# Kernel tuning notes

Measured on AMD Instinct MI355X. Metric: run time of the kernel, lower is better.

Reference implementation:

```python
import jax, jax.numpy as jnp
import numpy as np

B, M, N = 256, 256, 256

def setup_inputs() -> dict:
    key = jax.random.key(0)
    k1, k2 = jax.random.split(key)
    x_real = jax.random.normal(k1, (B, M, N), dtype=jnp.float32)
    x_imag = jax.random.normal(k2, (B, M, N), dtype=jnp.float32)
    return {"x_real": x_real, "x_imag": x_imag}

def reference(x_real, x_imag):
    # complex k-space input; original used complex128 via numpy on host,
    # we use complex64 (the natural accelerator precision), same math.
    x = jax.lax.complex(x_real, x_imag)  # [B, M, N]
    axes = (-2, -1)
    # centered 2D IFFT per sample (ifft_along_dim): fftshift(ifft2(ifftshift(x)))
    y = jnp.fft.fftshift(jnp.fft.ifft2(jnp.fft.ifftshift(x, axes=axes), axes=axes), axes=axes)
    y = y.reshape(-1, 1, M, N)  # (-1, 1, M, N) as in call()
    return (jnp.real(y), jnp.imag(y))
```

## Files before the change

kernel.cpp:

```cpp
#include <hip/hip_runtime.h>

namespace {

constexpr int NN  = 256;
constexpr int BMN = 256 * 256 * 256;

struct cpx { float re, im; };

__device__ __forceinline__ cpx cadd(cpx a, cpx b){ return cpx{a.re + b.re, a.im + b.im}; }
__device__ __forceinline__ cpx csub(cpx a, cpx b){ return cpx{a.re - b.re, a.im - b.im}; }
__device__ __forceinline__ cpx cmul(cpx a, cpx b){ return cpx{a.re*b.re - a.im*b.im, a.re*b.im + a.im*b.re}; }
__device__ __forceinline__ cpx cmuli(cpx a){ return cpx{-a.im, a.re}; }

__device__ __forceinline__ void r4(cpx a, cpx b, cpx c, cpx d,
                                   cpx& y0, cpx& y1, cpx& y2, cpx& y3) {
  cpx apc = cadd(a, c), amc = csub(a, c);
  cpx bpd = cadd(b, d), bmd = csub(b, d);
  cpx ib  = cmuli(bmd);
  y0 = cadd(apc, bpd);
  y1 = cadd(amc, ib);
  y2 = csub(apc, bpd);
  y3 = csub(amc, ib);
}

__device__ __forceinline__ void ifft16(cpx x[16]) {
  constexpr float WC[10] = { 1.f,  0.9238795325112867f,  0.7071067811865476f,  0.3826834323650898f, 0.f,
                            -0.3826834323650898f, -0.7071067811865476f, -0.9238795325112867f, -1.f,
                            -0.9238795325112867f };
  constexpr float WS[10] = { 0.f,  0.3826834323650898f,  0.7071067811865476f,  0.9238795325112867f, 1.f,
                             0.9238795325112867f,  0.7071067811865476f,  0.3826834323650898f,  0.f,
                            -0.3826834323650898f };
  cpx B[4][4];
#pragma unroll
  for (int n1 = 0; n1 < 4; ++n1)
    r4(x[n1], x[n1 + 4], x[n1 + 8], x[n1 + 12],
       B[n1][0], B[n1][1], B[n1][2], B[n1][3]);
#pragma unroll
  for (int n1 = 1; n1 < 4; ++n1)
#pragma unroll
    for (int k2 = 1; k2 < 4; ++k2)
      B[n1][k2] = cmul(B[n1][k2], cpx{WC[n1 * k2], WS[n1 * k2]});
#pragma unroll
  for (int k2 = 0; k2 < 4; ++k2)
    r4(B[0][k2], B[1][k2], B[2][k2], B[3][k2],
       x[k2], x[k2 + 4], x[k2 + 8], x[k2 + 12]);
}

__device__ __forceinline__ void twiddle256(cpx a[16], int t) {
  const float base = 0.024543692606170259f * (float)t;
#pragma unroll
  for (int k1 = 1; k1 < 16; ++k1) {
    float s, c;
    __sincosf(base * (float)k1, &s, &c);
    a[k1] = cmul(a[k1], cpx{c, s});
  }
}

__device__ __forceinline__ void transpose16(cpx a[16], float* L, int t) {
#pragma unroll
  for (int k1 = 0; k1 < 16; ++k1) L[k1 * 17 + t] = a[k1].re;
  __syncthreads();
  float br[16];
#pragma unroll
  for (int n2 = 0; n2 < 16; ++n2) br[n2] = L[t * 17 + n2];
  __syncthreads();
#pragma unroll
  for (int k1 = 0; k1 < 16; ++k1) L[k1 * 17 + t] = a[k1].im;
  __syncthreads();
#pragma unroll
  for (int n2 = 0; n2 < 16; ++n2) { a[n2].im = L[t * 17 + n2]; a[n2].re = br[n2]; }
}

__global__ __launch_bounds__(256)
void k_ifft_rows(const float* __restrict__ xr, const float* __restrict__ xi,
                 float* __restrict__ yr, float* __restrict__ yi) {
  __shared__ float lbuf[16 * 273];
  const int tid  = threadIdx.x;
  const int t    = tid & 15;
  const int ll   = tid >> 4;
  const int line = blockIdx.x * 16 + ll;
  const float* pr = xr + line * NN;
  const float* pi = xi + line * NN;

  cpx a[16];
#pragma unroll
  for (int j = 0; j < 16; ++j) {
    const int idx = (((j << 4) | t) ^ 128);
    a[j] = cpx{ pr[idx], pi[idx] };
  }
  ifft16(a);
  twiddle256(a, t);

  transpose16(a, lbuf + ll * 273, t);

  ifft16(a);
  float* qr = yr + line * NN;
  float* qi = yi + line * NN;
#pragma unroll
  for (int k = 0; k < 16; ++k) {
    const int idx = (((k << 4) | t) ^ 128);
    qr[idx] = a[k].re;
    qi[idx] = a[k].im;
  }
}

__global__ __launch_bounds__(512)
void k_ifft_cols(float* __restrict__ yr, float* __restrict__ yi) {
  __shared__ float lbuf[32 * 273];
  const int tid = threadIdx.x;
  const int c   = tid & 31;
  const int t   = tid >> 5;
  const int b   = blockIdx.x >> 3;
  const int c0  = (blockIdx.x & 7) << 5;
  const int base = b * 65536 + c0 + c;

  cpx a[16];
#pragma unroll
  for (int j = 0; j < 16; ++j) {
    const int m = (((j << 4) | t) ^ 128);
    a[j] = cpx{ yr[base + m * NN], yi[base + m * NN] };
  }
  ifft16(a);
  twiddle256(a, t);

  transpose16(a, lbuf + c * 273, t);

  ifft16(a);
  constexpr float sc = 1.0f / 65536.0f;
#pragma unroll
  for (int k = 0; k < 16; ++k) {
    const int m = (((k << 4) | t) ^ 128);
    yr[base + m * NN] = a[k].re * sc;
    yi[base + m * NN] = a[k].im * sc;
  }
}

}

extern "C" void kernel_launch(void* const* d_in, const int* in_sizes, int n_in,
                              void* d_out, int out_size, void* d_ws, size_t ws_size,
                              hipStream_t stream) {
  const float* xr = (const float*)d_in[0];
  const float* xi = (const float*)d_in[1];
  float* yr = (float*)d_out;
  float* yi = yr + BMN;

  k_ifft_rows<<<4096, 256, 0, stream>>>(xr, xi, yr, yi);
  k_ifft_cols<<<2048, 512, 0, stream>>>(yr, yi);
}
```

Baseline: 86.95 us.

## Stage row-FFT loads and stores through LDS with float4 coalesced access

The row kernel now loads its 16 lines with coalesced float4 global reads into padded shared buffers for real and imaginary parts, then gathers the shifted strided elements from LDS. Output goes back through LDS and is written with float4 stores. The internal transpose uses separate real/imag buffers, cutting one barrier round-trip. The aim is to replace strided 4-byte global accesses with wide coalesced ones, at the cost of more LDS traffic and extra barriers. The column kernel only has its transpose helper inlined.

```diff
diff --git a/kernel.cpp b/kernel.cpp
--- a/kernel.cpp
+++ b/kernel.cpp
@@ -2,8 +2,9 @@
 
 namespace {
 
-constexpr int NN  = 256;
-constexpr int BMN = 256 * 256 * 256;
+constexpr int NN   = 256;
+constexpr int BMN  = 256 * 256 * 256;
+constexpr int LPAD = 272;
 
 struct cpx { float re, im; };
 
@@ -56,51 +57,76 @@
   }
 }
 
-__device__ __forceinline__ void transpose16(cpx a[16], float* L, int t) {
-#pragma unroll
-  for (int k1 = 0; k1 < 16; ++k1) L[k1 * 17 + t] = a[k1].re;
-  __syncthreads();
-  float br[16];
-#pragma unroll
-  for (int n2 = 0; n2 < 16; ++n2) br[n2] = L[t * 17 + n2];
-  __syncthreads();
-#pragma unroll
-  for (int k1 = 0; k1 < 16; ++k1) L[k1 * 17 + t] = a[k1].im;
-  __syncthreads();
-#pragma unroll
-  for (int n2 = 0; n2 < 16; ++n2) { a[n2].im = L[t * 17 + n2]; a[n2].re = br[n2]; }
-}
-
 __global__ __launch_bounds__(256)
 void k_ifft_rows(const float* __restrict__ xr, const float* __restrict__ xi,
                  float* __restrict__ yr, float* __restrict__ yi) {
-  __shared__ float lbuf[16 * 273];
-  const int tid  = threadIdx.x;
-  const int t    = tid & 15;
-  const int ll   = tid >> 4;
-  const int line = blockIdx.x * 16 + ll;
-  const float* pr = xr + line * NN;
-  const float* pi = xi + line * NN;
+  __shared__ float Lr[16 * LPAD];
+  __shared__ float Li[16 * LPAD];
+  const int tid = threadIdx.x;
+  const int t   = tid & 15;
+  const int ll  = tid >> 4;
+
+  const size_t blk = (size_t)blockIdx.x * (16 * NN);
+  const float4* sr4 = reinterpret_cast<const float4*>(xr + blk);
+  const float4* si4 = reinterpret_cast<const float4*>(xi + blk);
+
+#pragma unroll
+  for (int q = 0; q < 4; ++q) {
+    const int fi   = (q << 8) + tid;
+    const int line = fi >> 6;
+    const int slot = fi & 63;
+    *reinterpret_cast<float4*>(&Lr[line * LPAD + slot * 4]) = sr4[fi];
+    *reinterpret_cast<float4*>(&Li[line * LPAD + slot * 4]) = si4[fi];
+  }
+  __syncthreads();
 
   cpx a[16];
+  {
+    const float* lr = Lr + ll * LPAD;
+    const float* li = Li + ll * LPAD;
 #pragma unroll
-  for (int j = 0; j < 16; ++j) {
-    const int idx = (((j << 4) | t) ^ 128);
-    a[j] = cpx{ pr[idx], pi[idx] };
+    for (int j = 0; j < 16; ++j) {
+      const int idx = (((j << 4) | t) ^ 128);
+      a[j] = cpx{ lr[idx], li[idx] };
+    }
   }
   ifft16(a);
   twiddle256(a, t);
+  __syncthreads();
 
-  transpose16(a, lbuf + ll * 273, t);
+  {
+    float* lr = Lr + ll * LPAD;
+    float* li = Li + ll * LPAD;
+#pragma unroll
+    for (int k1 = 0; k1 < 16; ++k1) { lr[k1 * 17 + t] = a[k1].re; li[k1 * 17 + t] = a[k1].im; }
+    __syncthreads();
+#pragma unroll
+    for (int n2 = 0; n2 < 16; ++n2) { a[n2].re = lr[t * 17 + n2]; a[n2].im = li[t * 17 + n2]; }
+  }
+  ifft16(a);
+  __syncthreads();
 
-  ifft16(a);
-  float* qr = yr + line * NN;
-  float* qi = yi + line * NN;
+  {
+    float* lr = Lr + ll * LPAD;
+    float* li = Li + ll * LPAD;
 #pragma unroll
-  for (int k = 0; k < 16; ++k) {
-    const int idx = (((k << 4) | t) ^ 128);
-    qr[idx] = a[k].re;
-    qi[idx] = a[k].im;
+    for (int k = 0; k < 16; ++k) {
+      const int idx = (((k << 4) | t) ^ 128);
+      lr[idx] = a[k].re;
+      li[idx] = a[k].im;
+    }
+  }
+  __syncthreads();
+
+  float4* dr4 = reinterpret_cast<float4*>(yr + blk);
+  float4* di4 = reinterpret_cast<float4*>(yi + blk);
+#pragma unroll
+  for (int q = 0; q < 4; ++q) {
+    const int fi   = (q << 8) + tid;
+    const int line = fi >> 6;
+    const int slot = fi & 63;
+    dr4[fi] = *reinterpret_cast<const float4*>(&Lr[line * LPAD + slot * 4]);
+    di4[fi] = *reinterpret_cast<const float4*>(&Li[line * LPAD + slot * 4]);
   }
 }
 
@@ -123,7 +149,21 @@
   ifft16(a);
   twiddle256(a, t);
 
-  transpose16(a, lbuf + c * 273, t);
+  {
+    float* L = lbuf + c * 273;
+#pragma unroll
+    for (int k1 = 0; k1 < 16; ++k1) L[k1 * 17 + t] = a[k1].re;
+    __syncthreads();
+    float br[16];
+#pragma unroll
+    for (int n2 = 0; n2 < 16; ++n2) br[n2] = L[t * 17 + n2];
+    __syncthreads();
+#pragma unroll
+    for (int k1 = 0; k1 < 16; ++k1) L[k1 * 17 + t] = a[k1].im;
+    __syncthreads();
+#pragma unroll
+    for (int n2 = 0; n2 < 16; ++n2) { a[n2].im = L[t * 17 + n2]; a[n2].re = br[n2]; }
+  }
 
   ifft16(a);
   constexpr float sc = 1.0f / 65536.0f;
```

New measurement: 86.54 us. About the same (-0.5%).
